# Performance work log

Hardware: AMD Instinct MI355X
Metric: run time of the kernel (lower is better)

The kernel has to match this reference:

```python
import jax, jax.numpy as jnp
import numpy as np

N = 100000      # nodes
E = 1600000     # edges (avg degree 16)
D_IN, D_HID, D_OUT = 128, 64, 32


def setup_inputs() -> dict:
    key = jax.random.key(0)
    ks = jax.random.split(key, 11)
    g = lambda k, shape, fan: jax.random.normal(k, shape, jnp.float32) * (1.0 / np.sqrt(fan))
    return {
        "x": jax.random.normal(ks[0], (N, D_IN), jnp.float32),
        "edges_index": jax.random.randint(ks[1], (2, E), 0, N, dtype=jnp.int64),
        # GATConv layer 1 (heads=1): linear weight, attention vectors a_src/a_dst, bias
        "W1": g(ks[2], (D_IN, D_HID), D_IN),
        "a_src1": g(ks[3], (D_HID,), D_HID),
        "a_dst1": g(ks[4], (D_HID,), D_HID),
        "b1": jnp.zeros((D_HID,), jnp.float32),
        # GATConv layer 2
        "W2": g(ks[5], (D_HID, D_OUT), D_HID),
        "a_src2": g(ks[6], (D_OUT,), D_OUT),
        "a_dst2": g(ks[7], (D_OUT,), D_OUT),
        "b2": jnp.zeros((D_OUT,), jnp.float32),
    }


def _gat_conv(x, src, dst, W, a_src, a_dst, b, n):
    """Single-head PyG GATConv: transform, edge attention, per-dst softmax, scatter-add."""
    h = x @ W                                        # [N, D]
    e = jax.nn.leaky_relu((h @ a_src)[src] + (h @ a_dst)[dst], 0.2)  # [E']
    # segment softmax over edges grouped by destination node
    m = jax.ops.segment_max(e, dst, num_segments=n)  # [N]
    w = jnp.exp(e - m[dst])                          # [E']
    s = jax.ops.segment_sum(w, dst, num_segments=n)  # [N]
    att = w / (s[dst] + 1e-16)                       # [E']
    out = jax.ops.segment_sum(att[:, None] * h[src], dst, num_segments=n)  # [N, D]
    return out + b


def reference(x, edges_index, W1, a_src1, a_dst1, b1, W2, a_src2, a_dst2, b2):
    n = x.shape[0]
    loops = jnp.arange(n, dtype=edges_index.dtype)   # GATConv add_self_loops=True
    src = jnp.concatenate([edges_index[0], loops])
    dst = jnp.concatenate([edges_index[1], loops])
    h = jax.nn.relu(_gat_conv(x, src, dst, W1, a_src1, a_dst1, b1, n))
    # F.dropout with training=False is identity (eval mode)
    out = _gat_conv(h, src, dst, W2, a_src2, a_dst2, b2, n)
    return jax.nn.log_softmax(out, axis=1)
```

## Files before the change

kernel.cpp:

```cpp
#include <hip/hip_runtime.h>
#include <math.h>

#define D_IN 128
#define D_HID 64
#define D_OUT 32
#define CAP 48
#define BSH 8
#define NB 391
#define CAPB 4608
#define CHUNK 8192

__device__ __forceinline__ unsigned short f2bf(float f) {
    unsigned u = __float_as_uint(f);
    unsigned r = (u + 0x7fffu + ((u >> 16) & 1u)) >> 16;
    return (unsigned short)r;
}
__device__ __forceinline__ float bf2f(unsigned short b) {
    return __uint_as_float(((unsigned)b) << 16);
}


__global__ __launch_bounds__(256) void init_kernel(
    int* __restrict__ cnt, int* __restrict__ cursor, int n)
{
    int i = blockIdx.x * 256 + threadIdx.x;
    if (i < n) cnt[i] = 0;
    if (i < NB) cursor[i] = i * CAPB;
}

__global__ __launch_bounds__(256) void part_kernel(
    const int* __restrict__ esrc, const int* __restrict__ edst,
    unsigned long long* __restrict__ ebuf, int* __restrict__ cursor,
    int E, int Et)
{
    __shared__ int hist[NB];
    __shared__ int ofs[NB];
    const int t = threadIdx.x;
    const int base = blockIdx.x * CHUNK;
    const int end = min(base + CHUNK, Et);

    for (int b = t; b < NB; b += 256) hist[b] = 0;
    __syncthreads();
    for (int i = base + t; i < end; i += 256) {
        int d = (i < E) ? edst[i] : (i - E);
        atomicAdd(&hist[d >> BSH], 1);
    }
    __syncthreads();
    for (int b = t; b < NB; b += 256) {
        int c = hist[b];
        ofs[b] = c ? atomicAdd(&cursor[b], c) : 0;
    }
    __syncthreads();
    for (int i = base + t; i < end; i += 256) {
        int d = (i < E) ? edst[i] : (i - E);
        int s = (i < E) ? esrc[i] : (i - E);
        int p = atomicAdd(&ofs[d >> BSH], 1);
        ebuf[p] = ((unsigned long long)(unsigned)s << 32) | (unsigned)d;
    }
}

__global__ __launch_bounds__(256) void fill_bucket_kernel(
    const unsigned long long* __restrict__ ebuf, const int* __restrict__ cursor,
    int* __restrict__ cnt, int* __restrict__ csr_pad)
{
    int b = blockIdx.x;
    int beg = b * CAPB;
    int end = cursor[b];
    for (int i = beg + threadIdx.x; i < end; i += 256) {
        unsigned long long v = ebuf[i];
        int d = (int)(v & 0xffffffffu);
        int s = (int)(v >> 32);
        int slot = atomicAdd(&cnt[d], 1);
        if (slot < CAP) csr_pad[(size_t)d * CAP + slot] = s;
    }
}


template<int K, int NC, int RT, int PAD>
__global__ __launch_bounds__(256) void gemm_alpha_kernel(
    const float* __restrict__ A, const float* __restrict__ W,
    const float* __restrict__ a_src, const float* __restrict__ a_dst,
    unsigned short* __restrict__ C, float* __restrict__ as_,
    float* __restrict__ ad_, int M)
{
    constexpr int TM = 64;
    constexpr int CT = 4;
    constexpr int CG = NC / CT;
    constexpr int KS = K + PAD;
    __shared__ float xs[TM * KS];
    __shared__ float ws[K * NC];
    const int t = threadIdx.x;

    for (int i = t; i < K * NC / 4; i += 256)
        ((float4*)ws)[i] = ((const float4*)W)[i];

    const int base = blockIdx.x * TM;
    for (int i = t; i < TM * K / 4; i += 256) {
        int nloc = i / (K / 4);
        int k4   = i % (K / 4);
        int row  = base + nloc;
        float4 v = make_float4(0.f, 0.f, 0.f, 0.f);
        if (row < M)
            v = *(const float4*)(A + (size_t)row * K + k4 * 4);
        *(float4*)(xs + nloc * KS + k4 * 4) = v;
    }
    __syncthreads();

    const int tx = t % CG, ty = t / CG;
    const int r0 = ty * RT, c0 = tx * CT;
    float acc[RT][CT];
#pragma unroll
    for (int i = 0; i < RT; ++i)
#pragma unroll
        for (int j = 0; j < CT; ++j) acc[i][j] = 0.f;

    for (int k = 0; k < K; k += 4) {
        float4 a[RT];
#pragma unroll
        for (int i = 0; i < RT; ++i)
            a[i] = *(const float4*)(xs + (r0 + i) * KS + k);
#pragma unroll
        for (int kk = 0; kk < 4; ++kk) {
            float4 b = *(const float4*)(ws + (k + kk) * NC + c0);
#pragma unroll
            for (int i = 0; i < RT; ++i) {
                float av = kk == 0 ? a[i].x : kk == 1 ? a[i].y :
                           kk == 2 ? a[i].z : a[i].w;
                acc[i][0] = fmaf(av, b.x, acc[i][0]);
                acc[i][1] = fmaf(av, b.y, acc[i][1]);
                acc[i][2] = fmaf(av, b.z, acc[i][2]);
                acc[i][3] = fmaf(av, b.w, acc[i][3]);
            }
        }
    }

    const float4 asv = *(const float4*)(a_src + c0);
    const float4 adv = *(const float4*)(a_dst + c0);
#pragma unroll
    for (int i = 0; i < RT; ++i) {
        int row = base + r0 + i;
        float ps = acc[i][0] * asv.x + acc[i][1] * asv.y +
                   acc[i][2] * asv.z + acc[i][3] * asv.w;
        float pd = acc[i][0] * adv.x + acc[i][1] * adv.y +
                   acc[i][2] * adv.z + acc[i][3] * adv.w;
#pragma unroll
        for (int o = 1; o < CG; o <<= 1) {
            ps += __shfl_xor(ps, o);
            pd += __shfl_xor(pd, o);
        }
        if (row < M) {
            ushort4 cv;
            cv.x = f2bf(acc[i][0]); cv.y = f2bf(acc[i][1]);
            cv.z = f2bf(acc[i][2]); cv.w = f2bf(acc[i][3]);
            *(ushort4*)(C + (size_t)row * NC + c0) = cv;
            if (tx == 0) { as_[row] = ps; ad_[row] = pd; }
        }
    }
}

__global__ __launch_bounds__(256) void gat_aggr_fused_kernel(
    const int* __restrict__ cnt, const int* __restrict__ csr_pad,
    const float* __restrict__ as1, const float* __restrict__ ad1,
    const unsigned short* __restrict__ h1, const float* __restrict__ b1,
    const float* __restrict__ W2, const float* __restrict__ a2s,
    const float* __restrict__ a2d, unsigned short* __restrict__ h2,
    float* __restrict__ as2, float* __restrict__ ad2, int n)
{
    __shared__ float w2s[D_HID * D_OUT];
    __shared__ float a2sv[D_OUT], a2dv[D_OUT];
    __shared__ float rbuf[4][64];
    const int t = threadIdx.x;
    for (int i = t; i < D_HID * D_OUT / 4; i += 256)
        ((float4*)w2s)[i] = ((const float4*)W2)[i];
    if (t < D_OUT) { a2sv[t] = a2s[t]; a2dv[t] = a2d[t]; }
    __syncthreads();

    int wave = t >> 6;
    int lane = t & 63;
    int d = blockIdx.x * 4 + wave;
    if (d >= n) return;
    int deg = min(cnt[d], CAP);
    float add = ad1[d];

    int s = 0; float e = -1e30f;
    if (lane < deg) {
        s = csr_pad[(size_t)d * CAP + lane];
        e = as1[s] + add;
        e = (e > 0.f) ? e : 0.2f * e;
    }
    float m = e;
#pragma unroll
    for (int o = 32; o > 0; o >>= 1) m = fmaxf(m, __shfl_xor(m, o));
    float w = __expf(e - m);
    float ssum = w;

    const int sub = lane >> 4;
    const unsigned short* hq = h1 + (lane & 15) * 4;
    float a0 = 0.f, a1 = 0.f, a2 = 0.f, a3 = 0.f;
    for (int tt = 0; tt < deg; tt += 16) {
        int i0 = tt + sub;
        const bool gB = tt + 4 < deg, gC = tt + 8 < deg, gD = tt + 12 < deg;
        float wA = __shfl(w, i0);      int sA = __shfl(s, i0);
        float wB = 0.f, wC = 0.f, wD = 0.f;
        int   sB = 0,   sC = 0,   sD = 0;
        ushort4 hA = *(const ushort4*)(hq + (size_t)sA * 64);
        ushort4 hB, hC, hD;
        if (gB) { wB = __shfl(w, i0 + 4);  sB = __shfl(s, i0 + 4);
                  hB = *(const ushort4*)(hq + (size_t)sB * 64); }
        if (gC) { wC = __shfl(w, i0 + 8);  sC = __shfl(s, i0 + 8);
                  hC = *(const ushort4*)(hq + (size_t)sC * 64); }
        if (gD) { wD = __shfl(w, i0 + 12); sD = __shfl(s, i0 + 12);
                  hD = *(const ushort4*)(hq + (size_t)sD * 64); }
        a0 = fmaf(wA, bf2f(hA.x), a0);
        a1 = fmaf(wA, bf2f(hA.y), a1);
        a2 = fmaf(wA, bf2f(hA.z), a2);
        a3 = fmaf(wA, bf2f(hA.w), a3);
        if (gB) {
            a0 = fmaf(wB, bf2f(hB.x), a0);
            a1 = fmaf(wB, bf2f(hB.y), a1);
            a2 = fmaf(wB, bf2f(hB.z), a2);
            a3 = fmaf(wB, bf2f(hB.w), a3);
        }
        if (gC) {
            a0 = fmaf(wC, bf2f(hC.x), a0);
            a1 = fmaf(wC, bf2f(hC.y), a1);
            a2 = fmaf(wC, bf2f(hC.z), a2);
            a3 = fmaf(wC, bf2f(hC.w), a3);
        }
        if (gD) {
            a0 = fmaf(wD, bf2f(hD.x), a0);
            a1 = fmaf(wD, bf2f(hD.y), a1);
            a2 = fmaf(wD, bf2f(hD.z), a2);
            a3 = fmaf(wD, bf2f(hD.w), a3);
        }
    }
#pragma unroll
    for (int o = 16; o <= 32; o <<= 1) {
        a0 += __shfl_xor(a0, o); a1 += __shfl_xor(a1, o);
        a2 += __shfl_xor(a2, o); a3 += __shfl_xor(a3, o);
    }
#pragma unroll
    for (int o = 32; o > 0; o >>= 1) ssum += __shfl_xor(ssum, o);

    float inv = 1.0f / (ssum + 1e-16f);
    const int q4 = (lane & 15) * 4;
    const float4 b1v = *(const float4*)(b1 + q4);
    float4 rv;
    rv.x = fmaxf(fmaf(a0, inv, b1v.x), 0.f);
    rv.y = fmaxf(fmaf(a1, inv, b1v.y), 0.f);
    rv.z = fmaxf(fmaf(a2, inv, b1v.z), 0.f);
    rv.w = fmaxf(fmaf(a3, inv, b1v.w), 0.f);
    if (sub == 0) *(float4*)(&rbuf[wave][q4]) = rv;

    int half = lane >> 5, j = lane & 31;
    const float* rb = &rbuf[wave][half * 32];
    const float* wp = w2s + (size_t)half * 32 * D_OUT + j;
    float acc2 = 0.f;
#pragma unroll
    for (int k = 0; k < 32; ++k)
        acc2 = fmaf(rb[k], wp[(size_t)k * D_OUT], acc2);
    acc2 += __shfl_xor(acc2, 32);

    float p1 = acc2 * a2sv[j], p2 = acc2 * a2dv[j];
#pragma unroll
    for (int o = 16; o > 0; o >>= 1) {
        p1 += __shfl_xor(p1, o);
        p2 += __shfl_xor(p2, o);
    }
    if (lane < 32) h2[(size_t)d * 32 + j] = f2bf(acc2);
    if (lane == 0) { as2[d] = p1; ad2[d] = p2; }
}

__global__ __launch_bounds__(256) void gat_aggr32_lsm_kernel(
    const int* __restrict__ cnt, const int* __restrict__ csr_pad,
    const float* __restrict__ as_, const float* __restrict__ ad_,
    const unsigned short* __restrict__ h, const float* __restrict__ bias,
    float* __restrict__ out, int n)
{
    int wave = threadIdx.x >> 6;
    int lane = threadIdx.x & 63;
    int d = blockIdx.x * 4 + wave;
    if (d >= n) return;
    int deg = min(cnt[d], CAP);
    float add = ad_[d];

    int s = 0; float e = -1e30f;
    if (lane < deg) {
        s = csr_pad[(size_t)d * CAP + lane];
        e = as_[s] + add;
        e = (e > 0.f) ? e : 0.2f * e;
    }
    float m = e;
#pragma unroll
    for (int o = 32; o > 0; o >>= 1) m = fmaxf(m, __shfl_xor(m, o));
    float w = __expf(e - m);
    float ssum = w;

    const int sub = lane >> 3;
    const unsigned short* hq = h + (lane & 7) * 4;
    float a0 = 0.f, a1 = 0.f, a2 = 0.f, a3 = 0.f;
    for (int tt = 0; tt < deg; tt += 16) {
        int i0 = tt + sub;
        const bool gB = tt + 8 < deg;
        float wA = __shfl(w, i0);  int sA = __shfl(s, i0);
        float wB = 0.f;            int sB = 0;
        ushort4 hA = *(const ushort4*)(hq + (size_t)sA * 32);
        ushort4 hB;
        if (gB) { wB = __shfl(w, i0 + 8); sB = __shfl(s, i0 + 8);
                  hB = *(const ushort4*)(hq + (size_t)sB * 32); }
        a0 = fmaf(wA, bf2f(hA.x), a0);
        a1 = fmaf(wA, bf2f(hA.y), a1);
        a2 = fmaf(wA, bf2f(hA.z), a2);
        a3 = fmaf(wA, bf2f(hA.w), a3);
        if (gB) {
            a0 = fmaf(wB, bf2f(hB.x), a0);
            a1 = fmaf(wB, bf2f(hB.y), a1);
            a2 = fmaf(wB, bf2f(hB.z), a2);
            a3 = fmaf(wB, bf2f(hB.w), a3);
        }
    }
#pragma unroll
    for (int o = 8; o <= 32; o <<= 1) {
        a0 += __shfl_xor(a0, o); a1 += __shfl_xor(a1, o);
        a2 += __shfl_xor(a2, o); a3 += __shfl_xor(a3, o);
    }
#pragma unroll
    for (int o = 32; o > 0; o >>= 1) ssum += __shfl_xor(ssum, o);

    float inv = 1.0f / (ssum + 1e-16f);
    const int q4 = (lane & 7) * 4;
    const float4 bv = *(const float4*)(bias + q4);
    float r0 = fmaf(a0, inv, bv.x), r1 = fmaf(a1, inv, bv.y);
    float r2 = fmaf(a2, inv, bv.z), r3 = fmaf(a3, inv, bv.w);

    float mx = fmaxf(fmaxf(r0, r1), fmaxf(r2, r3));
#pragma unroll
    for (int o = 1; o <= 4; o <<= 1) mx = fmaxf(mx, __shfl_xor(mx, o));
    float sm = __expf(r0 - mx) + __expf(r1 - mx) +
               __expf(r2 - mx) + __expf(r3 - mx);
#pragma unroll
    for (int o = 1; o <= 4; o <<= 1) sm += __shfl_xor(sm, o);
    float lg = mx + __logf(sm);
    if (sub == 0) {
        float4 ov = make_float4(r0 - lg, r1 - lg, r2 - lg, r3 - lg);
        *(float4*)(out + (size_t)d * 32 + q4) = ov;
    }
}

extern "C" void kernel_launch(void* const* d_in, const int* in_sizes, int n_in,
                              void* d_out, int out_size, void* d_ws, size_t ws_size,
                              hipStream_t stream) {
    const float* x    = (const float*)d_in[0];
    const int*   ei   = (const int*)  d_in[1];
    const float* W1   = (const float*)d_in[2];
    const float* av1s = (const float*)d_in[3];
    const float* av1d = (const float*)d_in[4];
    const float* b1   = (const float*)d_in[5];
    const float* W2   = (const float*)d_in[6];
    const float* av2s = (const float*)d_in[7];
    const float* av2d = (const float*)d_in[8];
    const float* b2   = (const float*)d_in[9];
    float* out = (float*)d_out;

    const int N  = in_sizes[0] / D_IN;
    const int E  = in_sizes[1] / 2;
    const int Et = E + N;
    const int* esrc = ei;
    const int* edst = ei + E;

    float* ws = (float*)d_ws;
    size_t off = 0;
    unsigned short* h1bf = (unsigned short*)(ws + off); off += (size_t)N * 32;
    unsigned short* h2bf = (unsigned short*)(ws + off); off += (size_t)N * 16;
    float* as1_ = ws + off;               off += N;
    float* ad1_ = ws + off;               off += N;
    float* as2_ = ws + off;               off += N;
    float* ad2_ = ws + off;               off += N;
    int* cnt    = (int*)(ws + off);       off += N;
    int* cursor = (int*)(ws + off);       off += NB + 1;
    int* csr_pad = (int*)(ws + off);      off += (size_t)N * CAP;
    if (off & 1) off++;
    unsigned long long* ebuf = (unsigned long long*)(ws + off);
    off += (size_t)NB * CAPB * 2;

    const int tiles  = (N + 63) / 64;
    const int nblk   = (N + 255) / 256;
    const int aggblk = (N + 3) / 4;
    const int pblk   = (Et + CHUNK - 1) / CHUNK;

    init_kernel<<<nblk, 256, 0, stream>>>(cnt, cursor, N);
    part_kernel<<<pblk, 256, 0, stream>>>(esrc, edst, ebuf, cursor, E, Et);
    fill_bucket_kernel<<<NB, 256, 0, stream>>>(ebuf, cursor, cnt, csr_pad);

    gemm_alpha_kernel<128, 64, 4, 0><<<tiles, 256, 0, stream>>>(
        x, W1, av1s, av1d, h1bf, as1_, ad1_, N);

    gat_aggr_fused_kernel<<<aggblk, 256, 0, stream>>>(
        cnt, csr_pad, as1_, ad1_, h1bf, b1,
        W2, av2s, av2d, h2bf, as2_, ad2_, N);

    gat_aggr32_lsm_kernel<<<aggblk, 256, 0, stream>>>(
        cnt, csr_pad, as2_, ad2_, h2bf, b2, out, N);
}
```

Measured before the change: 315.7 us.

## Switch intermediate features to fp16 with packed dot2 accumulation and persistent waves

Stores the hidden features h1/h2 as fp16 instead of bf16 and accumulates neighbour aggregation with packed fdot2 over pairs of edges, removing the per-element bf16 unpack and FMA chain. The layer-1 fused kernel now keeps the W2 column in registers rather than staging it in shared memory, and each wave processes four destination nodes to amortise that load. The gather loops are unrolled to issue all loads before the dot products, relying on padded zero-weight lanes. The changes lower precision on edge weights (packed to fp16 with round-toward-zero) and increase register pressure.

```diff
diff --git a/kernel.cpp b/kernel.cpp
--- a/kernel.cpp
+++ b/kernel.cpp
@@ -9,14 +9,46 @@
 #define NB 391
 #define CAPB 4608
 #define CHUNK 8192
-
-__device__ __forceinline__ unsigned short f2bf(float f) {
-    unsigned u = __float_as_uint(f);
-    unsigned r = (u + 0x7fffu + ((u >> 16) & 1u)) >> 16;
-    return (unsigned short)r;
-}
-__device__ __forceinline__ float bf2f(unsigned short b) {
-    return __uint_as_float(((unsigned)b) << 16);
+#define NPW 4
+
+typedef __fp16 half2f __attribute__((ext_vector_type(2)));
+
+__device__ __forceinline__ half2f u2h2(unsigned u) {
+    union { unsigned u; half2f h; } c; c.u = u; return c.h;
+}
+__device__ __forceinline__ unsigned h22u(half2f h) {
+    union { half2f h; unsigned u; } c; c.h = h; return c.u;
+}
+__device__ __forceinline__ unsigned short f2h(float f) {
+    union { _Float16 h; unsigned short u; } c; c.h = (_Float16)f; return c.u;
+}
+
+#if defined(__has_builtin)
+#  if __has_builtin(__builtin_amdgcn_fdot2)
+#    define HAVE_FDOT2 1
+#  else
+#    define HAVE_FDOT2 0
+#  endif
+#else
+#  define HAVE_FDOT2 0
+#endif
+
+__device__ __forceinline__ float fdot2f(half2f a, half2f b, float c) {
+#if HAVE_FDOT2
+    return __builtin_amdgcn_fdot2(a, b, c, false);
+#else
+    return fmaf((float)a.y, (float)b.y, fmaf((float)a.x, (float)b.x, c));
+#endif
+}
+
+__device__ __forceinline__ void pair_acc(float wA, float wB, uint2 hA, uint2 hB,
+                                         float& a0, float& a1, float& a2, float& a3)
+{
+    half2f wp = __builtin_amdgcn_cvt_pkrtz(wA, wB);
+    a0 = fdot2f(wp, u2h2(__builtin_amdgcn_perm(hB.x, hA.x, 0x05040100u)), a0);
+    a1 = fdot2f(wp, u2h2(__builtin_amdgcn_perm(hB.x, hA.x, 0x07060302u)), a1);
+    a2 = fdot2f(wp, u2h2(__builtin_amdgcn_perm(hB.y, hA.y, 0x05040100u)), a2);
+    a3 = fdot2f(wp, u2h2(__builtin_amdgcn_perm(hB.y, hA.y, 0x07060302u)), a3);
 }
 
 
@@ -149,10 +181,10 @@
             pd += __shfl_xor(pd, o);
         }
         if (row < M) {
-            ushort4 cv;
-            cv.x = f2bf(acc[i][0]); cv.y = f2bf(acc[i][1]);
-            cv.z = f2bf(acc[i][2]); cv.w = f2bf(acc[i][3]);
-            *(ushort4*)(C + (size_t)row * NC + c0) = cv;
+            uint2 cv;
+            cv.x = h22u(__builtin_amdgcn_cvt_pkrtz(acc[i][0], acc[i][1]));
+            cv.y = h22u(__builtin_amdgcn_cvt_pkrtz(acc[i][2], acc[i][3]));
+            *(uint2*)(C + (size_t)row * NC + c0) = cv;
             if (tx == 0) { as_[row] = ps; ad_[row] = pd; }
         }
     }
@@ -166,109 +198,124 @@
     const float* __restrict__ a2d, unsigned short* __restrict__ h2,
     float* __restrict__ as2, float* __restrict__ ad2, int n)
 {
-    __shared__ float w2s[D_HID * D_OUT];
-    __shared__ float a2sv[D_OUT], a2dv[D_OUT];
     __shared__ float rbuf[4][64];
     const int t = threadIdx.x;
-    for (int i = t; i < D_HID * D_OUT / 4; i += 256)
-        ((float4*)w2s)[i] = ((const float4*)W2)[i];
-    if (t < D_OUT) { a2sv[t] = a2s[t]; a2dv[t] = a2d[t]; }
-    __syncthreads();
-
-    int wave = t >> 6;
-    int lane = t & 63;
-    int d = blockIdx.x * 4 + wave;
-    if (d >= n) return;
-    int deg = min(cnt[d], CAP);
-    float add = ad1[d];
-
-    int s = 0; float e = -1e30f;
-    if (lane < deg) {
-        s = csr_pad[(size_t)d * CAP + lane];
-        e = as1[s] + add;
-        e = (e > 0.f) ? e : 0.2f * e;
-    }
-    float m = e;
-#pragma unroll
-    for (int o = 32; o > 0; o >>= 1) m = fmaxf(m, __shfl_xor(m, o));
-    float w = __expf(e - m);
-    float ssum = w;
+    const int wave = t >> 6;
+    const int lane = t & 63;
+    const int half = lane >> 5, j = lane & 31;
+
+    float w2r[32];
+#pragma unroll
+    for (int k = 0; k < 32; ++k)
+        w2r[k] = W2[(size_t)(half * 32 + k) * D_OUT + j];
+    const float a2sj = a2s[j], a2dj = a2d[j];
 
     const int sub = lane >> 4;
-    const unsigned short* hq = h1 + (lane & 15) * 4;
-    float a0 = 0.f, a1 = 0.f, a2 = 0.f, a3 = 0.f;
-    for (int tt = 0; tt < deg; tt += 16) {
-        int i0 = tt + sub;
-        const bool gB = tt + 4 < deg, gC = tt + 8 < deg, gD = tt + 12 < deg;
-        float wA = __shfl(w, i0);      int sA = __shfl(s, i0);
-        float wB = 0.f, wC = 0.f, wD = 0.f;
-        int   sB = 0,   sC = 0,   sD = 0;
-        ushort4 hA = *(const ushort4*)(hq + (size_t)sA * 64);
-        ushort4 hB, hC, hD;
-        if (gB) { wB = __shfl(w, i0 + 4);  sB = __shfl(s, i0 + 4);
-                  hB = *(const ushort4*)(hq + (size_t)sB * 64); }
-        if (gC) { wC = __shfl(w, i0 + 8);  sC = __shfl(s, i0 + 8);
-                  hC = *(const ushort4*)(hq + (size_t)sC * 64); }
-        if (gD) { wD = __shfl(w, i0 + 12); sD = __shfl(s, i0 + 12);
-                  hD = *(const ushort4*)(hq + (size_t)sD * 64); }
-        a0 = fmaf(wA, bf2f(hA.x), a0);
-        a1 = fmaf(wA, bf2f(hA.y), a1);
-        a2 = fmaf(wA, bf2f(hA.z), a2);
-        a3 = fmaf(wA, bf2f(hA.w), a3);
-        if (gB) {
-            a0 = fmaf(wB, bf2f(hB.x), a0);
-            a1 = fmaf(wB, bf2f(hB.y), a1);
-            a2 = fmaf(wB, bf2f(hB.z), a2);
-            a3 = fmaf(wB, bf2f(hB.w), a3);
-        }
-        if (gC) {
-            a0 = fmaf(wC, bf2f(hC.x), a0);
-            a1 = fmaf(wC, bf2f(hC.y), a1);
-            a2 = fmaf(wC, bf2f(hC.z), a2);
-            a3 = fmaf(wC, bf2f(hC.w), a3);
-        }
-        if (gD) {
-            a0 = fmaf(wD, bf2f(hD.x), a0);
-            a1 = fmaf(wD, bf2f(hD.y), a1);
-            a2 = fmaf(wD, bf2f(hD.z), a2);
-            a3 = fmaf(wD, bf2f(hD.w), a3);
-        }
-    }
-#pragma unroll
-    for (int o = 16; o <= 32; o <<= 1) {
-        a0 += __shfl_xor(a0, o); a1 += __shfl_xor(a1, o);
-        a2 += __shfl_xor(a2, o); a3 += __shfl_xor(a3, o);
-    }
-#pragma unroll
-    for (int o = 32; o > 0; o >>= 1) ssum += __shfl_xor(ssum, o);
-
-    float inv = 1.0f / (ssum + 1e-16f);
     const int q4 = (lane & 15) * 4;
+    const unsigned short* hq = h1 + q4;
     const float4 b1v = *(const float4*)(b1 + q4);
-    float4 rv;
-    rv.x = fmaxf(fmaf(a0, inv, b1v.x), 0.f);
-    rv.y = fmaxf(fmaf(a1, inv, b1v.y), 0.f);
-    rv.z = fmaxf(fmaf(a2, inv, b1v.z), 0.f);
-    rv.w = fmaxf(fmaf(a3, inv, b1v.w), 0.f);
-    if (sub == 0) *(float4*)(&rbuf[wave][q4]) = rv;
-
-    int half = lane >> 5, j = lane & 31;
-    const float* rb = &rbuf[wave][half * 32];
-    const float* wp = w2s + (size_t)half * 32 * D_OUT + j;
-    float acc2 = 0.f;
-#pragma unroll
-    for (int k = 0; k < 32; ++k)
-        acc2 = fmaf(rb[k], wp[(size_t)k * D_OUT], acc2);
-    acc2 += __shfl_xor(acc2, 32);
-
-    float p1 = acc2 * a2sv[j], p2 = acc2 * a2dv[j];
-#pragma unroll
-    for (int o = 16; o > 0; o >>= 1) {
-        p1 += __shfl_xor(p1, o);
-        p2 += __shfl_xor(p2, o);
-    }
-    if (lane < 32) h2[(size_t)d * 32 + j] = f2bf(acc2);
-    if (lane == 0) { as2[d] = p1; ad2[d] = p2; }
+
+    const int d0 = (blockIdx.x * 4 + wave) * NPW;
+    for (int it = 0; it < NPW; ++it) {
+        const int d = d0 + it;
+        if (d >= n) break;
+        const int deg = min(cnt[d], CAP);
+        const float add = ad1[d];
+
+        int s = 0; float e = -1e30f;
+        if (lane < deg) {
+            s = csr_pad[(size_t)d * CAP + lane];
+            float ev = as1[s] + add;
+            e = (ev > 0.f) ? ev : 0.2f * ev;
+        }
+        float m = e;
+#pragma unroll
+        for (int o = 32; o > 0; o >>= 1) m = fmaxf(m, __shfl_xor(m, o));
+        float w = __expf(e - m);
+        float ssum = w;
+
+        float a0 = 0.f, a1 = 0.f, a2v = 0.f, a3 = 0.f;
+        {
+            const int i0 = sub;
+            float wA = __shfl(w, i0),      wB = __shfl(w, i0 + 4);
+            float wC = __shfl(w, i0 + 8),  wD = __shfl(w, i0 + 12);
+            int   sA = __shfl(s, i0),      sB = __shfl(s, i0 + 4);
+            int   sC = __shfl(s, i0 + 8),  sD = __shfl(s, i0 + 12);
+            uint2 hA = *(const uint2*)(hq + (size_t)sA * 64);
+            uint2 hB = *(const uint2*)(hq + (size_t)sB * 64);
+            uint2 hC = *(const uint2*)(hq + (size_t)sC * 64);
+            uint2 hD = *(const uint2*)(hq + (size_t)sD * 64);
+            if (deg > 16) {
+                float wE = __shfl(w, i0 + 16), wF = __shfl(w, i0 + 20);
+                float wG = __shfl(w, i0 + 24), wH = __shfl(w, i0 + 28);
+                int   sE = __shfl(s, i0 + 16), sF = __shfl(s, i0 + 20);
+                int   sG = __shfl(s, i0 + 24), sH = __shfl(s, i0 + 28);
+                uint2 hE = *(const uint2*)(hq + (size_t)sE * 64);
+                uint2 hF = *(const uint2*)(hq + (size_t)sF * 64);
+                uint2 hG = *(const uint2*)(hq + (size_t)sG * 64);
+                uint2 hH = *(const uint2*)(hq + (size_t)sH * 64);
+                pair_acc(wA, wB, hA, hB, a0, a1, a2v, a3);
+                pair_acc(wC, wD, hC, hD, a0, a1, a2v, a3);
+                pair_acc(wE, wF, hE, hF, a0, a1, a2v, a3);
+                pair_acc(wG, wH, hG, hH, a0, a1, a2v, a3);
+            } else {
+                pair_acc(wA, wB, hA, hB, a0, a1, a2v, a3);
+                pair_acc(wC, wD, hC, hD, a0, a1, a2v, a3);
+            }
+        }
+        if (deg > 32) {
+            for (int tt = 32; tt < deg; tt += 16) {
+                const int i0 = tt + sub;
+                float wA = __shfl(w, i0),     wB = __shfl(w, i0 + 4);
+                float wC = __shfl(w, i0 + 8), wD = __shfl(w, i0 + 12);
+                int   sA = __shfl(s, i0),     sB = __shfl(s, i0 + 4);
+                int   sC = __shfl(s, i0 + 8), sD = __shfl(s, i0 + 12);
+                uint2 hA = *(const uint2*)(hq + (size_t)sA * 64);
+                uint2 hB = *(const uint2*)(hq + (size_t)sB * 64);
+                uint2 hC = *(const uint2*)(hq + (size_t)sC * 64);
+                uint2 hD = *(const uint2*)(hq + (size_t)sD * 64);
+                pair_acc(wA, wB, hA, hB, a0, a1, a2v, a3);
+                pair_acc(wC, wD, hC, hD, a0, a1, a2v, a3);
+            }
+        }
+
+#pragma unroll
+        for (int o = 16; o <= 32; o <<= 1) {
+            a0 += __shfl_xor(a0, o);  a1 += __shfl_xor(a1, o);
+            a2v += __shfl_xor(a2v, o); a3 += __shfl_xor(a3, o);
+        }
+#pragma unroll
+        for (int o = 32; o > 0; o >>= 1) ssum += __shfl_xor(ssum, o);
+
+        const float inv = 1.0f / (ssum + 1e-16f);
+        float4 rv;
+        rv.x = fmaxf(fmaf(a0, inv, b1v.x), 0.f);
+        rv.y = fmaxf(fmaf(a1, inv, b1v.y), 0.f);
+        rv.z = fmaxf(fmaf(a2v, inv, b1v.z), 0.f);
+        rv.w = fmaxf(fmaf(a3, inv, b1v.w), 0.f);
+        if (sub == 0) *(float4*)(&rbuf[wave][q4]) = rv;
+
+        const float* rb = &rbuf[wave][half * 32];
+        float acc2 = 0.f;
+#pragma unroll
+        for (int k4 = 0; k4 < 8; ++k4) {
+            float4 r4 = *(const float4*)(rb + k4 * 4);
+            acc2 = fmaf(r4.x, w2r[k4 * 4 + 0], acc2);
+            acc2 = fmaf(r4.y, w2r[k4 * 4 + 1], acc2);
+            acc2 = fmaf(r4.z, w2r[k4 * 4 + 2], acc2);
+            acc2 = fmaf(r4.w, w2r[k4 * 4 + 3], acc2);
+        }
+        acc2 += __shfl_xor(acc2, 32);
+
+        float p1 = acc2 * a2sj, p2 = acc2 * a2dj;
+#pragma unroll
+        for (int o = 16; o > 0; o >>= 1) {
+            p1 += __shfl_xor(p1, o);
+            p2 += __shfl_xor(p2, o);
+        }
+        if (lane < 32) h2[(size_t)d * 32 + j] = f2h(acc2);
+        if (lane == 0) { as2[d] = p1; ad2[d] = p2; }
+    }
 }
 
 __global__ __launch_bounds__(256) void gat_aggr32_lsm_kernel(
@@ -287,8 +334,8 @@
     int s = 0; float e = -1e30f;
     if (lane < deg) {
         s = csr_pad[(size_t)d * CAP + lane];
-        e = as_[s] + add;
-        e = (e > 0.f) ? e : 0.2f * e;
+        float ev = as_[s] + add;
+        e = (ev > 0.f) ? ev : 0.2f * ev;
     }
     float m = e;
 #pragma unroll
@@ -297,41 +344,48 @@
     float ssum = w;
 
     const int sub = lane >> 3;
-    const unsigned short* hq = h + (lane & 7) * 4;
-    float a0 = 0.f, a1 = 0.f, a2 = 0.f, a3 = 0.f;
-    for (int tt = 0; tt < deg; tt += 16) {
-        int i0 = tt + sub;
-        const bool gB = tt + 8 < deg;
-        float wA = __shfl(w, i0);  int sA = __shfl(s, i0);
-        float wB = 0.f;            int sB = 0;
-        ushort4 hA = *(const ushort4*)(hq + (size_t)sA * 32);
-        ushort4 hB;
-        if (gB) { wB = __shfl(w, i0 + 8); sB = __shfl(s, i0 + 8);
-                  hB = *(const ushort4*)(hq + (size_t)sB * 32); }
-        a0 = fmaf(wA, bf2f(hA.x), a0);
-        a1 = fmaf(wA, bf2f(hA.y), a1);
-        a2 = fmaf(wA, bf2f(hA.z), a2);
-        a3 = fmaf(wA, bf2f(hA.w), a3);
-        if (gB) {
-            a0 = fmaf(wB, bf2f(hB.x), a0);
-            a1 = fmaf(wB, bf2f(hB.y), a1);
-            a2 = fmaf(wB, bf2f(hB.z), a2);
-            a3 = fmaf(wB, bf2f(hB.w), a3);
+    const int q4 = (lane & 7) * 4;
+    const unsigned short* hq = h + q4;
+    float a0 = 0.f, a1 = 0.f, a2v = 0.f, a3 = 0.f;
+    {
+        const int i0 = sub;
+        float wA = __shfl(w, i0),      wB = __shfl(w, i0 + 8);
+        int   sA = __shfl(s, i0),      sB = __shfl(s, i0 + 8);
+        uint2 hA = *(const uint2*)(hq + (size_t)sA * 32);
+        uint2 hB = *(const uint2*)(hq + (size_t)sB * 32);
+        if (deg > 16) {
+            float wC = __shfl(w, i0 + 16), wD = __shfl(w, i0 + 24);
+            int   sC = __shfl(s, i0 + 16), sD = __shfl(s, i0 + 24);
+            uint2 hC = *(const uint2*)(hq + (size_t)sC * 32);
+            uint2 hD = *(const uint2*)(hq + (size_t)sD * 32);
+            pair_acc(wA, wB, hA, hB, a0, a1, a2v, a3);
+            pair_acc(wC, wD, hC, hD, a0, a1, a2v, a3);
+        } else {
+            pair_acc(wA, wB, hA, hB, a0, a1, a2v, a3);
+        }
+    }
+    if (deg > 32) {
+        for (int tt = 32; tt < deg; tt += 16) {
+            const int i0 = tt + sub;
+            float wA = __shfl(w, i0), wB = __shfl(w, i0 + 8);
+            int   sA = __shfl(s, i0), sB = __shfl(s, i0 + 8);
+            uint2 hA = *(const uint2*)(hq + (size_t)sA * 32);
+            uint2 hB = *(const uint2*)(hq + (size_t)sB * 32);
+            pair_acc(wA, wB, hA, hB, a0, a1, a2v, a3);
         }
     }
 #pragma unroll
     for (int o = 8; o <= 32; o <<= 1) {
-        a0 += __shfl_xor(a0, o); a1 += __shfl_xor(a1, o);
-        a2 += __shfl_xor(a2, o); a3 += __shfl_xor(a3, o);
+        a0 += __shfl_xor(a0, o);  a1 += __shfl_xor(a1, o);
+        a2v += __shfl_xor(a2v, o); a3 += __shfl_xor(a3, o);
     }
 #pragma unroll
     for (int o = 32; o > 0; o >>= 1) ssum += __shfl_xor(ssum, o);
 
     float inv = 1.0f / (ssum + 1e-16f);
-    const int q4 = (lane & 7) * 4;
     const float4 bv = *(const float4*)(bias + q4);
     float r0 = fmaf(a0, inv, bv.x), r1 = fmaf(a1, inv, bv.y);
-    float r2 = fmaf(a2, inv, bv.z), r3 = fmaf(a3, inv, bv.w);
+    float r2 = fmaf(a2v, inv, bv.z), r3 = fmaf(a3, inv, bv.w);
 
     float mx = fmaxf(fmaxf(r0, r1), fmaxf(r2, r3));
 #pragma unroll
@@ -370,8 +424,8 @@
 
     float* ws = (float*)d_ws;
     size_t off = 0;
-    unsigned short* h1bf = (unsigned short*)(ws + off); off += (size_t)N * 32;
-    unsigned short* h2bf = (unsigned short*)(ws + off); off += (size_t)N * 16;
+    unsigned short* h1f = (unsigned short*)(ws + off); off += (size_t)N * 32;
+    unsigned short* h2f_ = (unsigned short*)(ws + off); off += (size_t)N * 16;
     float* as1_ = ws + off;               off += N;
     float* ad1_ = ws + off;               off += N;
     float* as2_ = ws + off;               off += N;
@@ -386,6 +440,7 @@
     const int tiles  = (N + 63) / 64;
     const int nblk   = (N + 255) / 256;
     const int aggblk = (N + 3) / 4;
+    const int fblk   = (N + 4 * NPW - 1) / (4 * NPW);
     const int pblk   = (Et + CHUNK - 1) / CHUNK;
 
     init_kernel<<<nblk, 256, 0, stream>>>(cnt, cursor, N);
@@ -393,12 +448,12 @@
     fill_bucket_kernel<<<NB, 256, 0, stream>>>(ebuf, cursor, cnt, csr_pad);
 
     gemm_alpha_kernel<128, 64, 4, 0><<<tiles, 256, 0, stream>>>(
-        x, W1, av1s, av1d, h1bf, as1_, ad1_, N);
-
-    gat_aggr_fused_kernel<<<aggblk, 256, 0, stream>>>(
-        cnt, csr_pad, as1_, ad1_, h1bf, b1,
-        W2, av2s, av2d, h2bf, as2_, ad2_, N);
+        x, W1, av1s, av1d, h1f, as1_, ad1_, N);
+
+    gat_aggr_fused_kernel<<<fblk, 256, 0, stream>>>(
+        cnt, csr_pad, as1_, ad1_, h1f, b1,
+        W2, av2s, av2d, h2f_, as2_, ad2_, N);
 
     gat_aggr32_lsm_kernel<<<aggblk, 256, 0, stream>>>(
-        cnt, csr_pad, as2_, ad2_, h2bf, b2, out, N);
-}
+        cnt, csr_pad, as2_, ad2_, h2f_, b2, out, N);
+}
```

Result: no change. 311.6 us (-1.3%).
